# Performance work log

Hardware: AMD Instinct MI355X
Metric: run time of the kernel (lower is better)

## Reference

```python
import jax, jax.numpy as jnp
import numpy as np
from functools import partial

T0, T1, N = 0.0, 1.0, 1024
B = 131072
R, SIGMA = 0.1, 0.2


def setup_inputs() -> dict:
    key = jax.random.key(0)
    k0, k1 = jax.random.split(key)
    Z0 = jax.random.uniform(k0, (B,), dtype=jnp.float32) + 49.5  # around Z0=50 in source
    W = jax.random.normal(k1, (B, N + 1), dtype=jnp.float32)     # Brownian increments (W[:,0] unused)
    Wf = jnp.full((1, 1), R, dtype=jnp.float32)                  # drift weight (f = Linear 1x1)
    Wg = jnp.full((1, 1), SIGMA, dtype=jnp.float32)              # diffusion weight (g = Linear 1x1)
    return {"Z0": Z0, "W": W, "Wf": Wf, "Wg": Wg}


def reference(Z0, W, Wf, Wg):
    # Z[i+1] = Z[i] + f(Z[i])*dt + g(Z[i])*sqrt(dt)*W[i+1], f(z)=Wf*z, g(z)=Wg*z
    dt = jnp.float32((T1 - T0) / N)
    sdt = jnp.sqrt(dt)
    r = Wf[0, 0]
    s = Wg[0, 0]

    def step(z, w):  # z: [B], w: [B]
        zn = z + r * z * dt + s * z * sdt * w
        return zn, zn

    # scan over the N time steps; noise transposed to [N, B]
    _, Zs = jax.lax.scan(step, Z0, jnp.swapaxes(W[:, 1:], 0, 1))
    Z = jnp.concatenate([Z0[:, None], jnp.swapaxes(Zs, 0, 1)], axis=1)  # [B, N+1]
    return Z, W
```

## Files before the change

kernel.cpp:

```cpp
#include <hip/hip_runtime.h>


__global__ __launch_bounds__(256) void em_wave_kernel(
    const float* __restrict__ Z0,
    const float* __restrict__ W,
    const float* __restrict__ Wf,
    const float* __restrict__ Wg,
    float* __restrict__ Zout,
    float* __restrict__ Wout,
    int B)
{
    constexpr int NP1 = 1025;
    constexpr int NCH = 16;

    const int lane = threadIdx.x & 63;
    const int wid  = threadIdx.x >> 6;
    const int r    = blockIdx.x * 4 + wid;
    if (r >= B) return;

    const float dt  = 1.0f / 1024.0f;
    const float sdt = 0.03125f;
    const float a   = Wf[0] * dt;
    const float c   = Wg[0] * sdt;
    const float m0  = 1.0f + a;

    const size_t base = (size_t)r * NP1;
    const float* __restrict__ wrow  = W    + base;
    float*       __restrict__ zrow  = Zout + base;
    float*       __restrict__ worow = Wout + base;

    float w[NCH];
    #pragma unroll
    for (int k = 0; k < NCH; ++k)
        w[k] = wrow[1 + 64 * k + lane];

    #pragma unroll
    for (int k = 0; k < NCH; ++k)
        worow[1 + 64 * k + lane] = w[k];

    const float z0 = Z0[r];
    if (lane == 0) {
        zrow[0]  = z0;
        worow[0] = wrow[0];
    }

    float p[NCH];
    #pragma unroll
    for (int k = 0; k < NCH; ++k) {
        float v = fmaf(c, w[k], m0);
        #pragma unroll
        for (int d = 1; d < 64; d <<= 1) {
            float o = __shfl_up(v, d, 64);
            if (lane >= d) v *= o;
        }
        p[k] = v;
    }

    float carry = z0;
    #pragma unroll
    for (int k = 0; k < NCH; ++k) {
        zrow[1 + 64 * k + lane] = carry * p[k];
        carry *= __shfl(p[k], 63, 64);
    }
}

extern "C" void kernel_launch(void* const* d_in, const int* in_sizes, int n_in,
                              void* d_out, int out_size, void* d_ws, size_t ws_size,
                              hipStream_t stream) {
    const float* Z0 = (const float*)d_in[0];
    const float* W  = (const float*)d_in[1];
    const float* Wf = (const float*)d_in[2];
    const float* Wg = (const float*)d_in[3];

    const int B   = in_sizes[0];
    const int NP1 = in_sizes[1] / B;
    (void)NP1;

    float* Zout = (float*)d_out;
    float* Wout = Zout + (size_t)B * 1025;

    const int rowsPerBlock = 4;
    const int blocks = (B + rowsPerBlock - 1) / rowsPerBlock;
    em_wave_kernel<<<blocks, 256, 0, stream>>>(Z0, W, Wf, Wg, Zout, Wout, B);
}
```

Measured before the change: 325.5 us.

## Process one row per block with aligned float4 loads and block-level product scan

Each 256-thread block now handles one full row instead of one wavefront per row. Each thread loads an aligned float4 of noise after a scalar head and tail that fix the odd 1025-float row stride, and the per-row product is formed with a wave shuffle scan plus a shared-memory combine across the four waves. Block indices are also permuted so that consecutive blocks touch rows far apart in memory. The goal is wider, fewer memory transactions for this bandwidth-bound copy-and-scan, at the cost of a __syncthreads, scalar head and tail paths, and four times as many blocks.

```diff
diff --git a/kernel.cpp b/kernel.cpp
--- a/kernel.cpp
+++ b/kernel.cpp
@@ -1,7 +1,7 @@
 #include <hip/hip_runtime.h>
 
 
-__global__ __launch_bounds__(256) void em_wave_kernel(
+__global__ __launch_bounds__(256) void em_f4_kernel(
     const float* __restrict__ Z0,
     const float* __restrict__ W,
     const float* __restrict__ Wf,
@@ -11,12 +11,13 @@
     int B)
 {
     constexpr int NP1 = 1025;
-    constexpr int NCH = 16;
+    const int t    = threadIdx.x;
+    const int lane = t & 63;
+    const int wid  = t >> 6;
 
-    const int lane = threadIdx.x & 63;
-    const int wid  = threadIdx.x >> 6;
-    const int r    = blockIdx.x * 4 + wid;
-    if (r >= B) return;
+    const int nper = B >> 3;
+    const int bid  = (int)blockIdx.x;
+    const int r    = (bid & 7) * nper + (bid >> 3);
 
     const float dt  = 1.0f / 1024.0f;
     const float sdt = 0.03125f;
@@ -29,38 +30,81 @@
     float*       __restrict__ zrow  = Zout + base;
     float*       __restrict__ worow = Wout + base;
 
-    float w[NCH];
+    const int h    = (4 - ((r + 1) & 3)) & 3;
+    const int nv   = (1024 - h) >> 2;
+    const int tail = 1024 - h - (nv << 2);
+
+    float wh0 = 0.f, wh1 = 0.f, wh2 = 0.f;
+    float headprod = 1.0f;
+    if (h > 0) { wh0 = wrow[1]; headprod *= fmaf(c, wh0, m0); }
+    if (h > 1) { wh1 = wrow[2]; headprod *= fmaf(c, wh1, m0); }
+    if (h > 2) { wh2 = wrow[3]; headprod *= fmaf(c, wh2, m0); }
+
+    const bool isvec = (t < nv);
+    float4 wq = make_float4(0.f, 0.f, 0.f, 0.f);
+    float tw0 = 0.f, tw1 = 0.f, tw2 = 0.f;
+    float m1 = 1.f, m2 = 1.f, m3 = 1.f, m4 = 1.f;
+    const int i0 = 1 + h + (nv << 2);
+    if (isvec) {
+        const float4* __restrict__ wv =
+            reinterpret_cast<const float4*>(wrow + 1 + h);
+        wq = wv[t];
+        m1 = fmaf(c, wq.x, m0);
+        m2 = fmaf(c, wq.y, m0);
+        m3 = fmaf(c, wq.z, m0);
+        m4 = fmaf(c, wq.w, m0);
+    } else {
+        if (tail > 0) { tw0 = wrow[i0 + 0]; m1 = fmaf(c, tw0, m0); }
+        if (tail > 1) { tw1 = wrow[i0 + 1]; m2 = fmaf(c, tw1, m0); }
+        if (tail > 2) { tw2 = wrow[i0 + 2]; m3 = fmaf(c, tw2, m0); }
+    }
+    float prod = (m1 * m2) * (m3 * m4);
+
+    float p = prod;
     #pragma unroll
-    for (int k = 0; k < NCH; ++k)
-        w[k] = wrow[1 + 64 * k + lane];
+    for (int d = 1; d < 64; d <<= 1) {
+        float o = __shfl_up(p, d, 64);
+        if (lane >= d) p *= o;
+    }
 
-    #pragma unroll
-    for (int k = 0; k < NCH; ++k)
-        worow[1 + 64 * k + lane] = w[k];
+    __shared__ float wtot[4];
+    if (lane == 63) wtot[wid] = p;
+    __syncthreads();
+
+    float ep = __shfl_up(p, 1, 64);
+    if (lane == 0) ep = 1.0f;
+    float wpre = 1.0f;
+    if (wid > 0) wpre *= wtot[0];
+    if (wid > 1) wpre *= wtot[1];
+    if (wid > 2) wpre *= wtot[2];
 
     const float z0 = Z0[r];
-    if (lane == 0) {
+
+    if (t == 0) {
         zrow[0]  = z0;
         worow[0] = wrow[0];
+        float run = z0;
+        if (h > 0) { run *= fmaf(c, wh0, m0); zrow[1] = run; worow[1] = wh0; }
+        if (h > 1) { run *= fmaf(c, wh1, m0); zrow[2] = run; worow[2] = wh1; }
+        if (h > 2) { run *= fmaf(c, wh2, m0); zrow[3] = run; worow[3] = wh2; }
     }
 
-    float p[NCH];
-    #pragma unroll
-    for (int k = 0; k < NCH; ++k) {
-        float v = fmaf(c, w[k], m0);
-        #pragma unroll
-        for (int d = 1; d < 64; d <<= 1) {
-            float o = __shfl_up(v, d, 64);
-            if (lane >= d) v *= o;
-        }
-        p[k] = v;
-    }
+    const float S = ((z0 * headprod) * wpre) * ep;
 
-    float carry = z0;
-    #pragma unroll
-    for (int k = 0; k < NCH; ++k) {
-        zrow[1 + 64 * k + lane] = carry * p[k];
-        carry *= __shfl(p[k], 63, 64);
+    if (isvec) {
+        float zx = S  * m1;
+        float zy = zx * m2;
+        float zz = zy * m3;
+        float zw = zz * m4;
+        float4* __restrict__ zv  = reinterpret_cast<float4*>(zrow  + 1 + h);
+        float4* __restrict__ wov = reinterpret_cast<float4*>(worow + 1 + h);
+        zv[t]  = make_float4(zx, zy, zz, zw);
+        wov[t] = wq;
+    } else {
+        float run = S;
+        if (tail > 0) { run *= m1; zrow[i0 + 0] = run; worow[i0 + 0] = tw0; }
+        if (tail > 1) { run *= m2; zrow[i0 + 1] = run; worow[i0 + 1] = tw1; }
+        if (tail > 2) { run *= m3; zrow[i0 + 2] = run; worow[i0 + 2] = tw2; }
     }
 }
 
@@ -79,7 +123,5 @@
     float* Zout = (float*)d_out;
     float* Wout = Zout + (size_t)B * 1025;
 
-    const int rowsPerBlock = 4;
-    const int blocks = (B + rowsPerBlock - 1) / rowsPerBlock;
-    em_wave_kernel<<<blocks, 256, 0, stream>>>(Z0, W, Wf, Wg, Zout, Wout, B);
+    em_f4_kernel<<<B, 256, 0, stream>>>(Z0, W, Wf, Wg, Zout, Wout, B);
 }
```

After: 286.8 us. 1.14x faster.

## Vectorize row processing with aligned float4 loads and block-wide product scan

Applied to the files above, without the earlier changes.

Each block now handles two rows, with 256 threads each owning four contiguous elements, so loads and stores use float4 after a scalar head that brings the odd 1025-float row stride to 16-byte alignment. The prefix product becomes a per-thread product of four, a wave shuffle scan, then a cross-wave combine through shared memory and a barrier, replacing 16 chunked scans per wave. Block IDs are remapped to interleave rows, and launch bounds request higher occupancy. The aim is fewer, wider memory transactions on a bandwidth-bound kernel, at the cost of head/tail branching and a block-level sync.

```diff
diff --git a/kernel.cpp b/kernel.cpp
--- a/kernel.cpp
+++ b/kernel.cpp
@@ -1,7 +1,7 @@
 #include <hip/hip_runtime.h>
 
 
-__global__ __launch_bounds__(256) void em_wave_kernel(
+__global__ __launch_bounds__(256, 8) void em_f4x2_kernel(
     const float* __restrict__ Z0,
     const float* __restrict__ W,
     const float* __restrict__ Wf,
@@ -11,12 +11,15 @@
     int B)
 {
     constexpr int NP1 = 1025;
-    constexpr int NCH = 16;
+    const int t    = threadIdx.x;
+    const int lane = t & 63;
+    const int wid  = t >> 6;
 
-    const int lane = threadIdx.x & 63;
-    const int wid  = threadIdx.x >> 6;
-    const int r    = blockIdx.x * 4 + wid;
-    if (r >= B) return;
+    const int P   = B >> 1;
+    const int npx = P >> 3;
+    const int bid = (int)blockIdx.x;
+    const int q   = (bid & 7) * npx + (bid >> 3);
+    const int r0  = q << 1;
 
     const float dt  = 1.0f / 1024.0f;
     const float sdt = 0.03125f;
@@ -24,43 +27,112 @@
     const float c   = Wg[0] * sdt;
     const float m0  = 1.0f + a;
 
-    const size_t base = (size_t)r * NP1;
-    const float* __restrict__ wrow  = W    + base;
-    float*       __restrict__ zrow  = Zout + base;
-    float*       __restrict__ worow = Wout + base;
+    __shared__ float wtot[2][4];
 
-    float w[NCH];
-    #pragma unroll
-    for (int k = 0; k < NCH; ++k)
-        w[k] = wrow[1 + 64 * k + lane];
+    float m[2][4];
+    float pincl[2];
+    float z0v[2], headprod[2];
+    int   hh[2], nvv[2], i0v[2], tlv[2];
 
     #pragma unroll
-    for (int k = 0; k < NCH; ++k)
-        worow[1 + 64 * k + lane] = w[k];
+    for (int j = 0; j < 2; ++j) {
+        const int r = r0 + j;
+        const size_t base = (size_t)r * NP1;
+        const float* __restrict__ wrow  = W    + base;
+        float*       __restrict__ worow = Wout + base;
+        float*       __restrict__ zrow  = Zout + base;
 
-    const float z0 = Z0[r];
-    if (lane == 0) {
-        zrow[0]  = z0;
-        worow[0] = wrow[0];
+        const int h  = (4 - ((r + 1) & 3)) & 3;
+        const int nv = (1024 - h) >> 2;
+        const int i0 = 1 + h + (nv << 2);
+        const int tl = 1024 - h - (nv << 2);
+        hh[j] = h; nvv[j] = nv; i0v[j] = i0; tlv[j] = tl;
+
+        float wh0 = 0.f, wh1 = 0.f, wh2 = 0.f;
+        if (h > 0) wh0 = wrow[1];
+        if (h > 1) wh1 = wrow[2];
+        if (h > 2) wh2 = wrow[3];
+
+        float mm0 = 1.f, mm1 = 1.f, mm2 = 1.f, mm3 = 1.f;
+        if (t < nv) {
+            const float4* __restrict__ wv =
+                reinterpret_cast<const float4*>(wrow + 1 + h);
+            float4 wq = wv[t];
+            mm0 = fmaf(c, wq.x, m0);
+            mm1 = fmaf(c, wq.y, m0);
+            mm2 = fmaf(c, wq.z, m0);
+            mm3 = fmaf(c, wq.w, m0);
+            float4* __restrict__ wov =
+                reinterpret_cast<float4*>(worow + 1 + h);
+            wov[t] = wq;
+        } else {
+            if (tl > 0) { float tw = wrow[i0+0]; mm0 = fmaf(c, tw, m0); worow[i0+0] = tw; }
+            if (tl > 1) { float tw = wrow[i0+1]; mm1 = fmaf(c, tw, m0); worow[i0+1] = tw; }
+            if (tl > 2) { float tw = wrow[i0+2]; mm2 = fmaf(c, tw, m0); worow[i0+2] = tw; }
+        }
+
+        const float z0 = Z0[r];
+        float hp = 1.0f;
+        if (h > 0) hp *= fmaf(c, wh0, m0);
+        if (h > 1) hp *= fmaf(c, wh1, m0);
+        if (h > 2) hp *= fmaf(c, wh2, m0);
+
+        if (t == 0) {
+            zrow[0]  = z0;
+            worow[0] = wrow[0];
+            float run = z0;
+            if (h > 0) { run *= fmaf(c, wh0, m0); zrow[1] = run; worow[1] = wh0; }
+            if (h > 1) { run *= fmaf(c, wh1, m0); zrow[2] = run; worow[2] = wh1; }
+            if (h > 2) { run *= fmaf(c, wh2, m0); zrow[3] = run; worow[3] = wh2; }
+        }
+
+        m[j][0] = mm0; m[j][1] = mm1; m[j][2] = mm2; m[j][3] = mm3;
+        z0v[j] = z0; headprod[j] = hp;
     }
 
-    float p[NCH];
     #pragma unroll
-    for (int k = 0; k < NCH; ++k) {
-        float v = fmaf(c, w[k], m0);
+    for (int j = 0; j < 2; ++j) {
+        float p = (m[j][0] * m[j][1]) * (m[j][2] * m[j][3]);
         #pragma unroll
         for (int d = 1; d < 64; d <<= 1) {
-            float o = __shfl_up(v, d, 64);
-            if (lane >= d) v *= o;
+            float o = __shfl_up(p, d, 64);
+            if (lane >= d) p *= o;
         }
-        p[k] = v;
+        pincl[j] = p;
+        if (lane == 63) wtot[j][wid] = p;
     }
 
-    float carry = z0;
+    __syncthreads();
+
     #pragma unroll
-    for (int k = 0; k < NCH; ++k) {
-        zrow[1 + 64 * k + lane] = carry * p[k];
-        carry *= __shfl(p[k], 63, 64);
+    for (int j = 0; j < 2; ++j) {
+        const int r = r0 + j;
+        const size_t base = (size_t)r * NP1;
+        float* __restrict__ zrow = Zout + base;
+
+        float ep = __shfl_up(pincl[j], 1, 64);
+        if (lane == 0) ep = 1.0f;
+        float wpre = 1.0f;
+        if (wid > 0) wpre *= wtot[j][0];
+        if (wid > 1) wpre *= wtot[j][1];
+        if (wid > 2) wpre *= wtot[j][2];
+
+        const float S = ((z0v[j] * headprod[j]) * wpre) * ep;
+        const int h = hh[j], nv = nvv[j], i0 = i0v[j], tl = tlv[j];
+
+        if (t < nv) {
+            float zx = S  * m[j][0];
+            float zy = zx * m[j][1];
+            float zz = zy * m[j][2];
+            float zw = zz * m[j][3];
+            float4* __restrict__ zv = reinterpret_cast<float4*>(zrow + 1 + h);
+            zv[t] = make_float4(zx, zy, zz, zw);
+        } else {
+            float run = S;
+            if (tl > 0) { run *= m[j][0]; zrow[i0 + 0] = run; }
+            if (tl > 1) { run *= m[j][1]; zrow[i0 + 1] = run; }
+            if (tl > 2) { run *= m[j][2]; zrow[i0 + 2] = run; }
+        }
     }
 }
 
@@ -79,7 +151,6 @@
     float* Zout = (float*)d_out;
     float* Wout = Zout + (size_t)B * 1025;
 
-    const int rowsPerBlock = 4;
-    const int blocks = (B + rowsPerBlock - 1) / rowsPerBlock;
-    em_wave_kernel<<<blocks, 256, 0, stream>>>(Z0, W, Wf, Wg, Zout, Wout, B);
+    const int blocks = B >> 1;
+    em_f4x2_kernel<<<blocks, 256, 0, stream>>>(Z0, W, Wf, Wg, Zout, Wout, B);
 }
```

After: 297.8 us. -8.5%, faster.
